# Kernel optimization log

Hardware: AMD Instinct MI355X
Metric: run time of the kernel (lower is better)

Reference implementation:

```python
import jax, jax.numpy as jnp
import numpy as np

B, S, D_MODEL, D_QK, D_VO = 4, 2048, 1024, 128, 128
NEG = -1.0e9


def setup_inputs() -> dict:
    key = jax.random.key(0)
    k1, k2, k3, k4, k5 = jax.random.split(key, 5)
    enc = jax.random.normal(k1, (B, S, D_MODEL), dtype=jnp.float32)
    # causal mask: True means masked (masked_fill), broadcast over batch
    causal = jnp.triu(jnp.ones((S, S), dtype=bool), k=1)
    mask = jnp.broadcast_to(causal, (B, S, S))
    scale = 0.02
    W_q = jax.random.normal(k2, (D_MODEL, D_QK), dtype=jnp.float32) * scale
    W_k = jax.random.normal(k3, (D_MODEL, D_QK), dtype=jnp.float32) * scale
    W_v = jax.random.normal(k4, (D_MODEL, D_VO), dtype=jnp.float32) * scale
    W_o = jax.random.normal(k5, (D_VO, D_MODEL), dtype=jnp.float32) * scale
    return {"encodings": enc, "mask": mask, "W_q": W_q, "W_k": W_k, "W_v": W_v, "W_o": W_o}


def reference(encodings, mask, W_q, W_k, W_v, W_o):
    # q,k: [B,S,d_qk]; v: [B,S,d_vo]
    q = jnp.einsum('bsd,de->bse', encodings, W_q)
    k = jnp.einsum('bsd,de->bse', encodings, W_k)
    v = jnp.einsum('bsd,de->bse', encodings, W_v)
    sims = jnp.einsum('bqe,bke->bqk', q, k) / jnp.asarray(D_QK ** 0.5, q.dtype)
    sims = jnp.where(mask, jnp.asarray(NEG, sims.dtype), sims)
    attn = jax.nn.softmax(sims, axis=-1)  # [B,S,S]
    scores = jnp.einsum('bqk,bke->bqe', attn, v)  # [B,S,d_vo]
    return jnp.einsum('bse,ed->bsd', scores, W_o)  # [B,S,d_model]
```

## Files before the change

### kernel.cpp

```cpp
#include <hip/hip_runtime.h>
#include <hip/hip_bf16.h>
#include <stdint.h>

typedef __attribute__((ext_vector_type(8))) short short8;
typedef __attribute__((ext_vector_type(4))) float floatx4;

using bf16 = __hip_bfloat16;

#define SCALE_L2 0.12751793359133147f

__device__ inline unsigned short f2b(float f) {
    bf16 h = __float2bfloat16(f);
    return *(unsigned short*)&h;
}
__device__ inline float b2f(unsigned short u) {
    union { unsigned int i; float f; } v;
    v.i = ((unsigned int)u) << 16;
    return v.f;
}

__device__ __forceinline__ void gll16(const bf16* g, bf16* l) {
    __builtin_amdgcn_global_load_lds((__attribute__((address_space(1))) void*)g,
                                     (__attribute__((address_space(3))) void*)l,
                                     16, 0, 0);
}

__global__ __launch_bounds__(256) void prep_all(const float4* __restrict__ enc4,
                                                ushort4* __restrict__ encb4,
                                                const float* __restrict__ Wq,
                                                const float* __restrict__ Wk,
                                                const float* __restrict__ Wv,
                                                const float* __restrict__ Wo,
                                                bf16* __restrict__ Wqkvt,
                                                bf16* __restrict__ Wot) {
    int bx = blockIdx.x;
    if (bx < 8192) {
        int i = bx * 256 + threadIdx.x;
        float4 v = enc4[i];
        ushort4 o;
        o.x = f2b(v.x); o.y = f2b(v.y); o.z = f2b(v.z); o.w = f2b(v.w);
        encb4[i] = o;
    } else {
        int idx = (bx - 8192) * 256 + threadIdx.x;
        int sel = idx >> 17;
        int i = idx & 131071;
        if (sel < 3) {
            const float* W = (sel == 0) ? Wq : (sel == 1) ? Wk : Wv;
            int r = i >> 7, c = i & 127;
            Wqkvt[(size_t)(sel * 128 + c) * 1024 + r] = __float2bfloat16(W[i]);
        } else {
            int r = i >> 10, c = i & 1023;
            Wot[(size_t)c * 128 + r] = __float2bfloat16(Wo[i]);
        }
    }
}

__global__ __launch_bounds__(256) void gemm_qkv(const bf16* __restrict__ A,
                                                const bf16* __restrict__ Bt,
                                                bf16* __restrict__ Qb,
                                                bf16* __restrict__ Kb,
                                                bf16* __restrict__ Vtb) {
    __shared__ bf16 As[64 * 32];
    __shared__ bf16 Bs[64 * 32];

    const int tid = threadIdx.x;
    const int m0 = blockIdx.x * 64;
    const int by = blockIdx.y;
    const int nsel = by >> 1;
    const int nh = by & 1;
    const int brow0 = nsel * 128 + nh * 64;
    const int w = tid >> 6, lane = tid & 63;
    const int wm = (w >> 1) * 32, wn = (w & 1) * 32;
    const int quad = lane >> 4, l16 = lane & 15;

    const int ar = tid >> 2, akq = (tid & 3) * 8;
    bf16* As_w = &As[w * 512];
    bf16* Bs_w = &Bs[w * 512];

    floatx4 acc[2][2];
#pragma unroll
    for (int i = 0; i < 2; i++)
#pragma unroll
        for (int j = 0; j < 2; j++) acc[i][j] = (floatx4){0.f, 0.f, 0.f, 0.f};

    for (int k0 = 0; k0 < 1024; k0 += 32) {
        __syncthreads();
        gll16(&A[(size_t)(m0 + ar) * 1024 + k0 + akq], As_w);
        gll16(&Bt[(size_t)(brow0 + ar) * 1024 + k0 + akq], Bs_w);
        __syncthreads();

        short8 a[2], b[2];
#pragma unroll
        for (int mt = 0; mt < 2; mt++)
            a[mt] = *(const short8*)&As[(wm + mt * 16 + l16) * 32 + quad * 8];
#pragma unroll
        for (int nt = 0; nt < 2; nt++)
            b[nt] = *(const short8*)&Bs[(wn + nt * 16 + l16) * 32 + quad * 8];
#pragma unroll
        for (int mt = 0; mt < 2; mt++)
#pragma unroll
            for (int nt = 0; nt < 2; nt++)
                acc[mt][nt] = __builtin_amdgcn_mfma_f32_16x16x32_bf16(a[mt], b[nt], acc[mt][nt], 0, 0, 0);
    }

#pragma unroll
    for (int mt = 0; mt < 2; mt++)
#pragma unroll
        for (int nt = 0; nt < 2; nt++)
#pragma unroll
            for (int r = 0; r < 4; r++) {
                int row = m0 + wm + mt * 16 + quad * 4 + r;
                int col = nh * 64 + wn + nt * 16 + l16;
                bf16 h = __float2bfloat16(acc[mt][nt][r]);
                if (nsel == 0) {
                    Qb[(size_t)row * 128 + col] = h;
                } else if (nsel == 1) {
                    Kb[(size_t)row * 128 + col] = h;
                } else {
                    int bb = row >> 11, ss = row & 2047;
                    Vtb[(size_t)bb * 262144 + (size_t)col * 2048 + ss] = h;
                }
            }
}

__global__ __launch_bounds__(256) void gemm_out(const bf16* __restrict__ A,
                                                const bf16* __restrict__ Bt,
                                                float* __restrict__ C) {
    __shared__ bf16 As[64 * 40];
    __shared__ bf16 Bs[128 * 40];

    const int tid = threadIdx.x;
    const int m0 = blockIdx.x * 64;
    const int n0 = blockIdx.y * 128;
    const int w = tid >> 6, lane = tid & 63;
    const int wm = (w >> 1) * 32, wn = (w & 1) * 64;
    const int quad = lane >> 4, l16 = lane & 15;

    const int ra = tid >> 2, ca = (tid & 3) * 8;
    const int rb0 = tid >> 2, rb1 = (tid + 256) >> 2;

    floatx4 acc[2][4];
#pragma unroll
    for (int i = 0; i < 2; i++)
#pragma unroll
        for (int j = 0; j < 4; j++) acc[i][j] = (floatx4){0.f, 0.f, 0.f, 0.f};

    int4 pa  = *(const int4*)&A[(size_t)(m0 + ra) * 128 + ca];
    int4 pb0 = *(const int4*)&Bt[(size_t)(n0 + rb0) * 128 + ca];
    int4 pb1 = *(const int4*)&Bt[(size_t)(n0 + rb1) * 128 + ca];

    for (int k0 = 0; k0 < 128; k0 += 32) {
        __syncthreads();
        *(int4*)&As[ra * 40 + ca] = pa;
        *(int4*)&Bs[rb0 * 40 + ca] = pb0;
        *(int4*)&Bs[rb1 * 40 + ca] = pb1;
        __syncthreads();

        if (k0 + 32 < 128) {
            pa  = *(const int4*)&A[(size_t)(m0 + ra) * 128 + k0 + 32 + ca];
            pb0 = *(const int4*)&Bt[(size_t)(n0 + rb0) * 128 + k0 + 32 + ca];
            pb1 = *(const int4*)&Bt[(size_t)(n0 + rb1) * 128 + k0 + 32 + ca];
        }

        short8 a[2], b[4];
#pragma unroll
        for (int mt = 0; mt < 2; mt++)
            a[mt] = *(const short8*)&As[(wm + mt * 16 + l16) * 40 + quad * 8];
#pragma unroll
        for (int nt = 0; nt < 4; nt++)
            b[nt] = *(const short8*)&Bs[(wn + nt * 16 + l16) * 40 + quad * 8];
#pragma unroll
        for (int mt = 0; mt < 2; mt++)
#pragma unroll
            for (int nt = 0; nt < 4; nt++)
                acc[mt][nt] = __builtin_amdgcn_mfma_f32_16x16x32_bf16(a[mt], b[nt], acc[mt][nt], 0, 0, 0);
    }

#pragma unroll
    for (int mt = 0; mt < 2; mt++)
#pragma unroll
        for (int nt = 0; nt < 4; nt++)
#pragma unroll
            for (int r = 0; r < 4; r++) {
                int row = m0 + wm + mt * 16 + quad * 4 + r;
                int col = n0 + wn + nt * 16 + l16;
                C[(size_t)row * 1024 + col] = acc[mt][nt][r];
            }
}

__global__ __launch_bounds__(64) void flash_split(const bf16* __restrict__ Q,
                                                  const bf16* __restrict__ K,
                                                  const bf16* __restrict__ Vt,
                                                  bf16* __restrict__ Opb,
                                                  float2* __restrict__ Ml) {
    __shared__ bf16 Pw[2176];

    const int tid = threadIdx.x;
    const int x = blockIdx.x;
    const int b = x / 1088;
    const int rr = x - b * 1088;
    const int id = rr >> 2;
    const int strip = rr & 3;
    int qt = (int)__builtin_amdgcn_sqrtf(4.0f * (float)id + 1.0f) - 1;
    if (qt < 0) qt = 0;
    while (((qt + 2) * (qt + 2)) / 4 <= id) qt++;
    while (((qt + 1) * (qt + 1)) / 4 > id) qt--;
    const int c = id - ((qt + 1) * (qt + 1)) / 4;
    const int q0 = qt * 64;
    const int start = 2 * c;
    const int end = min(start + 2, qt + 1);

    const int lane = tid;
    const int quad = lane >> 4, l16 = lane & 15;
    bf16* myP = Pw;

    const int qrow = q0 + strip * 16 + l16;
    const bf16* Qrow = &Q[((size_t)b * 2048 + qrow) * 128];
    short8 qf[4];
#pragma unroll
    for (int k4 = 0; k4 < 4; k4++)
        qf[k4] = *(const short8*)&Qrow[k4 * 32 + quad * 8];

    const bf16* Kl = &K[((size_t)b * 2048 + l16) * 128 + quad * 8];
    const bf16* Vl = &Vt[(size_t)b * 262144 + (size_t)l16 * 2048 + quad * 8];

    float m_run = -1.0e30f, l_run = 0.f;
    floatx4 o[8];
#pragma unroll
    for (int d = 0; d < 8; d++) o[d] = (floatx4){0.f, 0.f, 0.f, 0.f};

    for (int kt = start; kt < end; kt++) {
        short8 kc[16];
#pragma unroll
        for (int nt = 0; nt < 4; nt++)
#pragma unroll
            for (int k4 = 0; k4 < 4; k4++)
                kc[nt * 4 + k4] = *(const short8*)&Kl[(size_t)(kt * 64 + nt * 16) * 128 + k4 * 32];

        floatx4 s_acc[4];
#pragma unroll
        for (int nt = 0; nt < 4; nt++) {
            s_acc[nt] = (floatx4){0.f, 0.f, 0.f, 0.f};
#pragma unroll
            for (int k4 = 0; k4 < 4; k4++)
                s_acc[nt] = __builtin_amdgcn_mfma_f32_16x16x32_bf16(kc[nt * 4 + k4], qf[k4], s_acc[nt], 0, 0, 0);
        }

        float sv[4][4];
#pragma unroll
        for (int nt = 0; nt < 4; nt++)
#pragma unroll
            for (int r = 0; r < 4; r++) {
                float s = s_acc[nt][r] * SCALE_L2;
                if (kt == qt) {
                    int kcol = kt * 64 + nt * 16 + quad * 4 + r;
                    if (kcol > qrow) s = -1.0e9f;
                }
                sv[nt][r] = s;
            }

        float t0 = fmaxf(fmaxf(sv[0][0], sv[0][1]), fmaxf(sv[0][2], sv[0][3]));
        float t1 = fmaxf(fmaxf(sv[1][0], sv[1][1]), fmaxf(sv[1][2], sv[1][3]));
        float t2 = fmaxf(fmaxf(sv[2][0], sv[2][1]), fmaxf(sv[2][2], sv[2][3]));
        float t3 = fmaxf(fmaxf(sv[3][0], sv[3][1]), fmaxf(sv[3][2], sv[3][3]));
        float tmax = fmaxf(fmaxf(t0, t1), fmaxf(t2, t3));
        tmax = fmaxf(tmax, __shfl_xor(tmax, 16));
        tmax = fmaxf(tmax, __shfl_xor(tmax, 32));

        float mnew = fmaxf(m_run, tmax);
        float alpha = exp2f(m_run - mnew);
        m_run = mnew;

        float rsum = 0.f;
#pragma unroll
        for (int nt = 0; nt < 4; nt++)
#pragma unroll
            for (int r = 0; r < 4; r++) {
                float p = exp2f(sv[nt][r] - mnew);
                sv[nt][r] = p;
                rsum += p;
            }
        rsum += __shfl_xor(rsum, 16);
        rsum += __shfl_xor(rsum, 32);
        l_run = l_run * alpha + rsum;

#pragma unroll
        for (int nt = 0; nt < 4; nt++) {
            ushort4 pk;
            pk.x = f2b(sv[nt][0]); pk.y = f2b(sv[nt][1]);
            pk.z = f2b(sv[nt][2]); pk.w = f2b(sv[nt][3]);
            *(ushort4*)&myP[l16 * 72 + nt * 16 + quad * 4] = pk;
        }

#pragma unroll
        for (int d = 0; d < 8; d++) {
            o[d][0] *= alpha; o[d][1] *= alpha; o[d][2] *= alpha; o[d][3] *= alpha;
        }

        short8 pf[2];
#pragma unroll
        for (int k2 = 0; k2 < 2; k2++)
            pf[k2] = *(const short8*)&myP[l16 * 72 + k2 * 32 + quad * 8];
#pragma unroll
        for (int d = 0; d < 8; d++)
#pragma unroll
            for (int k2 = 0; k2 < 2; k2++) {
                short8 vf = *(const short8*)&Vl[(size_t)(d * 16) * 2048 + kt * 64 + k2 * 32];
                o[d] = __builtin_amdgcn_mfma_f32_16x16x32_bf16(vf, pf[k2], o[d], 0, 0, 0);
            }
    }

#pragma unroll
    for (int d = 0; d < 8; d++) {
        ushort4 pk;
        pk.x = f2b(o[d][0]); pk.y = f2b(o[d][1]);
        pk.z = f2b(o[d][2]); pk.w = f2b(o[d][3]);
        *(ushort4*)&myP[l16 * 136 + d * 16 + quad * 4] = pk;
    }
    const int chunk = b * 272 + id;
    const int er = lane >> 2;
    const int ec = lane & 3;
    const size_t orow = ((size_t)chunk * 64 + strip * 16 + er) * 128;
#pragma unroll
    for (int p = 0; p < 4; p++) {
        int ce = (p * 4 + ec) * 8;
        short8 t = *(const short8*)&myP[er * 136 + ce];
        *(short8*)&Opb[orow + ce] = t;
    }
    if (lane < 16) Ml[(size_t)chunk * 64 + strip * 16 + l16] = make_float2(m_run, l_run);
}

__global__ __launch_bounds__(256) void flash_merge(const bf16* __restrict__ Opb,
                                                   const float2* __restrict__ Ml,
                                                   bf16* __restrict__ Sc) {
    int idx = blockIdx.x * 256 + threadIdx.x;
    int row = idx >> 5, dg = (idx & 31) * 4;
    int b = row >> 11, s = row & 2047;
    int qt = s >> 6, rl = s & 63;
    int nc = (qt >> 1) + 1;
    int id0 = b * 272 + ((qt + 1) * (qt + 1)) / 4;

    float M = -1.0e30f;
    for (int j = 0; j < nc; j++)
        M = fmaxf(M, Ml[(size_t)(id0 + j) * 64 + rl].x);

    float L = 0.f;
    float a0 = 0.f, a1 = 0.f, a2 = 0.f, a3 = 0.f;
    for (int j = 0; j < nc; j++) {
        float2 t = Ml[(size_t)(id0 + j) * 64 + rl];
        float wj = exp2f(t.x - M);
        L += t.y * wj;
        ushort4 p = *(const ushort4*)&Opb[((size_t)(id0 + j) * 64 + rl) * 128 + dg];
        a0 += wj * b2f(p.x); a1 += wj * b2f(p.y);
        a2 += wj * b2f(p.z); a3 += wj * b2f(p.w);
    }
    float inv = 1.0f / L;
    ushort4 o;
    o.x = f2b(a0 * inv); o.y = f2b(a1 * inv);
    o.z = f2b(a2 * inv); o.w = f2b(a3 * inv);
    *(ushort4*)&Sc[(size_t)row * 128 + dg] = o;
}

extern "C" void kernel_launch(void* const* d_in, const int* in_sizes, int n_in,
                              void* d_out, int out_size, void* d_ws, size_t ws_size,
                              hipStream_t stream) {
    const float* enc = (const float*)d_in[0];
    const float* Wq = (const float*)d_in[2];
    const float* Wk = (const float*)d_in[3];
    const float* Wv = (const float*)d_in[4];
    const float* Wo = (const float*)d_in[5];
    float* out = (float*)d_out;

    const size_t MB = 1024 * 1024;
    char* ws = (char*)d_ws;
    bf16*   Qb    = (bf16*)(ws);
    bf16*   Kb    = (bf16*)(ws + 2 * MB);
    bf16*   Vtb   = (bf16*)(ws + 4 * MB);
    bf16*   Scb   = (bf16*)(ws + 6 * MB);
    bf16*   Wqkvt = (bf16*)(ws + 8 * MB);
    bf16*   Wot   = (bf16*)(ws + 8 * MB + 768 * 1024);
    float2* Ml    = (float2*)(ws + 9 * MB);
    bf16*   encb  = (bf16*)(ws + 10 * MB);
    bf16*   Opb   = (bf16*)(ws + 10 * MB);

    prep_all<<<10240, 256, 0, stream>>>((const float4*)enc, (ushort4*)encb,
                                        Wq, Wk, Wv, Wo, Wqkvt, Wot);

    gemm_qkv<<<dim3(128, 6), dim3(256), 0, stream>>>(encb, Wqkvt, Qb, Kb, Vtb);

    flash_split<<<4352, dim3(64), 0, stream>>>(Qb, Kb, Vtb, Opb, Ml);
    flash_merge<<<1024, dim3(256), 0, stream>>>(Opb, Ml, Scb);

    gemm_out<<<dim3(128, 8), dim3(256), 0, stream>>>(Scb, Wot, out);
}
```

Baseline: 204.1 us.

## Fuse encoder bf16 cast into QKV GEMM and share K/V tiles in LDS

The separate pass that converts the encoder input to bf16 is removed. The QKV GEMM now reads fp32 encodings directly, converts them in registers and writes them to LDS, prefetching the next k-slice into registers. The flash split kernel changes from four 64-thread blocks per chunk to one 256-thread block whose four waves share swizzled K and V tiles loaded into LDS with global_load_lds, instead of each wave loading K and V from global memory itself. This cuts a full read-write of the encoder tensor and repeated K/V global traffic, at the cost of extra block-level barriers and higher LDS use per block.

```diff
diff --git a/kernel.cpp b/kernel.cpp
--- a/kernel.cpp
+++ b/kernel.cpp
@@ -25,43 +25,32 @@
                                      16, 0, 0);
 }
 
-__global__ __launch_bounds__(256) void prep_all(const float4* __restrict__ enc4,
-                                                ushort4* __restrict__ encb4,
-                                                const float* __restrict__ Wq,
-                                                const float* __restrict__ Wk,
-                                                const float* __restrict__ Wv,
-                                                const float* __restrict__ Wo,
-                                                bf16* __restrict__ Wqkvt,
-                                                bf16* __restrict__ Wot) {
-    int bx = blockIdx.x;
-    if (bx < 8192) {
-        int i = bx * 256 + threadIdx.x;
-        float4 v = enc4[i];
-        ushort4 o;
-        o.x = f2b(v.x); o.y = f2b(v.y); o.z = f2b(v.z); o.w = f2b(v.w);
-        encb4[i] = o;
+__global__ __launch_bounds__(256) void prep_w(const float* __restrict__ Wq,
+                                              const float* __restrict__ Wk,
+                                              const float* __restrict__ Wv,
+                                              const float* __restrict__ Wo,
+                                              bf16* __restrict__ Wqkvt,
+                                              bf16* __restrict__ Wot) {
+    int idx = blockIdx.x * 256 + threadIdx.x;
+    int sel = idx >> 17;
+    int i = idx & 131071;
+    if (sel < 3) {
+        const float* W = (sel == 0) ? Wq : (sel == 1) ? Wk : Wv;
+        int r = i >> 7, c = i & 127;
+        Wqkvt[(size_t)(sel * 128 + c) * 1024 + r] = __float2bfloat16(W[i]);
     } else {
-        int idx = (bx - 8192) * 256 + threadIdx.x;
-        int sel = idx >> 17;
-        int i = idx & 131071;
-        if (sel < 3) {
-            const float* W = (sel == 0) ? Wq : (sel == 1) ? Wk : Wv;
-            int r = i >> 7, c = i & 127;
-            Wqkvt[(size_t)(sel * 128 + c) * 1024 + r] = __float2bfloat16(W[i]);
-        } else {
-            int r = i >> 10, c = i & 1023;
-            Wot[(size_t)c * 128 + r] = __float2bfloat16(Wo[i]);
-        }
-    }
-}
-
-__global__ __launch_bounds__(256) void gemm_qkv(const bf16* __restrict__ A,
+        int r = i >> 10, c = i & 1023;
+        Wot[(size_t)c * 128 + r] = __float2bfloat16(Wo[i]);
+    }
+}
+
+__global__ __launch_bounds__(256) void gemm_qkv(const float* __restrict__ enc,
                                                 const bf16* __restrict__ Bt,
                                                 bf16* __restrict__ Qb,
                                                 bf16* __restrict__ Kb,
                                                 bf16* __restrict__ Vtb) {
-    __shared__ bf16 As[64 * 32];
-    __shared__ bf16 Bs[64 * 32];
+    __shared__ __align__(16) bf16 As[64 * 32];
+    __shared__ __align__(16) bf16 Bs[64 * 32];
 
     const int tid = threadIdx.x;
     const int m0 = blockIdx.x * 64;
@@ -74,8 +63,11 @@
     const int quad = lane >> 4, l16 = lane & 15;
 
     const int ar = tid >> 2, akq = (tid & 3) * 8;
-    bf16* As_w = &As[w * 512];
     bf16* Bs_w = &Bs[w * 512];
+
+    const float4* Arow = (const float4*)&enc[(size_t)(m0 + ar) * 1024];
+    const int af = (tid & 3) * 2;
+    float4 a0 = Arow[af], a1 = Arow[af + 1];
 
     floatx4 acc[2][2];
 #pragma unroll
@@ -85,22 +77,31 @@
 
     for (int k0 = 0; k0 < 1024; k0 += 32) {
         __syncthreads();
-        gll16(&A[(size_t)(m0 + ar) * 1024 + k0 + akq], As_w);
         gll16(&Bt[(size_t)(brow0 + ar) * 1024 + k0 + akq], Bs_w);
+        ushort4 u0, u1;
+        u0.x = f2b(a0.x); u0.y = f2b(a0.y); u0.z = f2b(a0.z); u0.w = f2b(a0.w);
+        u1.x = f2b(a1.x); u1.y = f2b(a1.y); u1.z = f2b(a1.z); u1.w = f2b(a1.w);
+        *(ushort4*)&As[ar * 32 + akq] = u0;
+        *(ushort4*)&As[ar * 32 + akq + 4] = u1;
         __syncthreads();
 
-        short8 a[2], b[2];
+        if (k0 + 32 < 1024) {
+            a0 = Arow[((k0 + 32) >> 2) + af];
+            a1 = Arow[((k0 + 32) >> 2) + af + 1];
+        }
+
+        short8 a[2], bfr[2];
 #pragma unroll
         for (int mt = 0; mt < 2; mt++)
             a[mt] = *(const short8*)&As[(wm + mt * 16 + l16) * 32 + quad * 8];
 #pragma unroll
         for (int nt = 0; nt < 2; nt++)
-            b[nt] = *(const short8*)&Bs[(wn + nt * 16 + l16) * 32 + quad * 8];
+            bfr[nt] = *(const short8*)&Bs[(wn + nt * 16 + l16) * 32 + quad * 8];
 #pragma unroll
         for (int mt = 0; mt < 2; mt++)
 #pragma unroll
             for (int nt = 0; nt < 2; nt++)
-                acc[mt][nt] = __builtin_amdgcn_mfma_f32_16x16x32_bf16(a[mt], b[nt], acc[mt][nt], 0, 0, 0);
+                acc[mt][nt] = __builtin_amdgcn_mfma_f32_16x16x32_bf16(a[mt], bfr[nt], acc[mt][nt], 0, 0, 0);
     }
 
 #pragma unroll
@@ -188,19 +189,19 @@
             }
 }
 
-__global__ __launch_bounds__(64) void flash_split(const bf16* __restrict__ Q,
-                                                  const bf16* __restrict__ K,
-                                                  const bf16* __restrict__ Vt,
-                                                  bf16* __restrict__ Opb,
-                                                  float2* __restrict__ Ml) {
-    __shared__ bf16 Pw[2176];
+__global__ __launch_bounds__(256) void flash_split(const bf16* __restrict__ Q,
+                                                   const bf16* __restrict__ K,
+                                                   const bf16* __restrict__ Vt,
+                                                   bf16* __restrict__ Opb,
+                                                   float2* __restrict__ Ml) {
+    __shared__ __align__(16) bf16 Ks[64 * 128];
+    __shared__ __align__(16) bf16 Vs[128 * 64];
+    __shared__ __align__(16) bf16 Pw[4 * 2176];
 
     const int tid = threadIdx.x;
     const int x = blockIdx.x;
-    const int b = x / 1088;
-    const int rr = x - b * 1088;
-    const int id = rr >> 2;
-    const int strip = rr & 3;
+    const int b = x / 272;
+    const int id = x - b * 272;
     int qt = (int)__builtin_amdgcn_sqrtf(4.0f * (float)id + 1.0f) - 1;
     if (qt < 0) qt = 0;
     while (((qt + 2) * (qt + 2)) / 4 <= id) qt++;
@@ -210,40 +211,58 @@
     const int start = 2 * c;
     const int end = min(start + 2, qt + 1);
 
-    const int lane = tid;
+    const int w = tid >> 6, lane = tid & 63;
     const int quad = lane >> 4, l16 = lane & 15;
-    bf16* myP = Pw;
-
-    const int qrow = q0 + strip * 16 + l16;
+    bf16* myP = &Pw[w * 2176];
+
+    const int krow = w * 4 + (lane >> 4);
+    const int kcb  = (lane & 15) * 16;
+    const int vrow = w * 8 + (lane >> 3);
+    const int vcb  = (lane & 7) * 16;
+    const int ksw  = (l16 & 7) << 4;
+
+    const int qrow = q0 + w * 16 + l16;
     const bf16* Qrow = &Q[((size_t)b * 2048 + qrow) * 128];
     short8 qf[4];
 #pragma unroll
     for (int k4 = 0; k4 < 4; k4++)
         qf[k4] = *(const short8*)&Qrow[k4 * 32 + quad * 8];
 
-    const bf16* Kl = &K[((size_t)b * 2048 + l16) * 128 + quad * 8];
-    const bf16* Vl = &Vt[(size_t)b * 262144 + (size_t)l16 * 2048 + quad * 8];
-
     float m_run = -1.0e30f, l_run = 0.f;
     floatx4 o[8];
 #pragma unroll
     for (int d = 0; d < 8; d++) o[d] = (floatx4){0.f, 0.f, 0.f, 0.f};
 
+    {
+        const int kt = start;
+#pragma unroll
+        for (int i = 0; i < 4; i++) {
+            int row = i * 16 + krow;
+            int cbs = kcb ^ ((row & 7) << 4);
+            gll16(&K[((size_t)b * 2048 + kt * 64 + row) * 128 + (cbs >> 1)],
+                  &Ks[i * 2048 + w * 512]);
+        }
+#pragma unroll
+        for (int i = 0; i < 4; i++) {
+            int row = i * 32 + vrow;
+            int cbs = vcb ^ ((row & 7) << 4);
+            gll16(&Vt[(size_t)b * 262144 + (size_t)row * 2048 + kt * 64 + (cbs >> 1)],
+                  &Vs[i * 2048 + w * 512]);
+        }
+    }
+    __syncthreads();
+
     for (int kt = start; kt < end; kt++) {
-        short8 kc[16];
-#pragma unroll
-        for (int nt = 0; nt < 4; nt++)
-#pragma unroll
-            for (int k4 = 0; k4 < 4; k4++)
-                kc[nt * 4 + k4] = *(const short8*)&Kl[(size_t)(kt * 64 + nt * 16) * 128 + k4 * 32];
-
         floatx4 s_acc[4];
 #pragma unroll
         for (int nt = 0; nt < 4; nt++) {
             s_acc[nt] = (floatx4){0.f, 0.f, 0.f, 0.f};
 #pragma unroll
-            for (int k4 = 0; k4 < 4; k4++)
-                s_acc[nt] = __builtin_amdgcn_mfma_f32_16x16x32_bf16(kc[nt * 4 + k4], qf[k4], s_acc[nt], 0, 0, 0);
+            for (int k4 = 0; k4 < 4; k4++) {
+                short8 kf = *(const short8*)((const char*)Ks +
+                              (nt * 16 + l16) * 256 + ((k4 * 64 + quad * 16) ^ ksw));
+                s_acc[nt] = __builtin_amdgcn_mfma_f32_16x16x32_bf16(kf, qf[k4], s_acc[nt], 0, 0, 0);
+            }
         }
 
         float sv[4][4];
@@ -305,9 +324,30 @@
         for (int d = 0; d < 8; d++)
 #pragma unroll
             for (int k2 = 0; k2 < 2; k2++) {
-                short8 vf = *(const short8*)&Vl[(size_t)(d * 16) * 2048 + kt * 64 + k2 * 32];
+                short8 vf = *(const short8*)((const char*)Vs +
+                              (d * 16 + l16) * 128 + ((k2 * 64 + quad * 16) ^ ksw));
                 o[d] = __builtin_amdgcn_mfma_f32_16x16x32_bf16(vf, pf[k2], o[d], 0, 0, 0);
             }
+
+        if (kt + 1 < end) {
+            __syncthreads();
+            const int nk = kt + 1;
+#pragma unroll
+            for (int i = 0; i < 4; i++) {
+                int row = i * 16 + krow;
+                int cbs = kcb ^ ((row & 7) << 4);
+                gll16(&K[((size_t)b * 2048 + nk * 64 + row) * 128 + (cbs >> 1)],
+                      &Ks[i * 2048 + w * 512]);
+            }
+#pragma unroll
+            for (int i = 0; i < 4; i++) {
+                int row = i * 32 + vrow;
+                int cbs = vcb ^ ((row & 7) << 4);
+                gll16(&Vt[(size_t)b * 262144 + (size_t)row * 2048 + nk * 64 + (cbs >> 1)],
+                      &Vs[i * 2048 + w * 512]);
+            }
+            __syncthreads();
+        }
     }
 
 #pragma unroll
@@ -317,17 +357,16 @@
         pk.z = f2b(o[d][2]); pk.w = f2b(o[d][3]);
         *(ushort4*)&myP[l16 * 136 + d * 16 + quad * 4] = pk;
     }
-    const int chunk = b * 272 + id;
     const int er = lane >> 2;
     const int ec = lane & 3;
-    const size_t orow = ((size_t)chunk * 64 + strip * 16 + er) * 128;
+    const size_t orow = ((size_t)x * 64 + w * 16 + er) * 128;
 #pragma unroll
     for (int p = 0; p < 4; p++) {
         int ce = (p * 4 + ec) * 8;
         short8 t = *(const short8*)&myP[er * 136 + ce];
         *(short8*)&Opb[orow + ce] = t;
     }
-    if (lane < 16) Ml[(size_t)chunk * 64 + strip * 16 + l16] = make_float2(m_run, l_run);
+    if (lane < 16) Ml[(size_t)x * 64 + w * 16 + l16] = make_float2(m_run, l_run);
 }
 
 __global__ __launch_bounds__(256) void flash_merge(const bf16* __restrict__ Opb,
@@ -380,15 +419,13 @@
     bf16*   Wqkvt = (bf16*)(ws + 8 * MB);
     bf16*   Wot   = (bf16*)(ws + 8 * MB + 768 * 1024);
     float2* Ml    = (float2*)(ws + 9 * MB);
-    bf16*   encb  = (bf16*)(ws + 10 * MB);
     bf16*   Opb   = (bf16*)(ws + 10 * MB);
 
-    prep_all<<<10240, 256, 0, stream>>>((const float4*)enc, (ushort4*)encb,
-                                        Wq, Wk, Wv, Wo, Wqkvt, Wot);
-
-    gemm_qkv<<<dim3(128, 6), dim3(256), 0, stream>>>(encb, Wqkvt, Qb, Kb, Vtb);
-
-    flash_split<<<4352, dim3(64), 0, stream>>>(Qb, Kb, Vtb, Opb, Ml);
+    prep_w<<<2048, dim3(256), 0, stream>>>(Wq, Wk, Wv, Wo, Wqkvt, Wot);
+
+    gemm_qkv<<<dim3(128, 6), dim3(256), 0, stream>>>(enc, Wqkvt, Qb, Kb, Vtb);
+
+    flash_split<<<1088, dim3(256), 0, stream>>>(Qb, Kb, Vtb, Opb, Ml);
     flash_merge<<<1024, dim3(256), 0, stream>>>(Opb, Ml, Scb);
 
     gemm_out<<<dim3(128, 8), dim3(256), 0, stream>>>(Scb, Wot, out);
```

Result: faster. 188.8 us (-7.5%).
